# Kernel optimization log

Hardware: AMD Instinct MI355X
Metric: run time of the kernel (lower is better)

## Reference

```python
import jax, jax.numpy as jnp
import numpy as np

# torch.optim.Adam defaults
LR = 1e-3
B1 = 0.9
B2 = 0.999
EPS = 1e-8


def setup_inputs() -> dict:
    key = jax.random.key(0)
    k1, k2 = jax.random.split(key)
    B, N_train, d = 128, 16384, 1024
    h = jax.random.normal(k1, (B, d), dtype=jnp.float32)
    H_train = jax.random.normal(k2, (N_train, d), dtype=jnp.float32)
    return {"h": h, "H_train": H_train, "n_epoch": 1000}


def reference(h, H_train, n_epoch):
    # preweights: [B, N_train], optimized by Adam for n_epoch steps
    B, N_train = h.shape[0], H_train.shape[0]

    def loss_fn(p):
        w = jax.nn.softmax(p, axis=-1)          # [B, N_train]
        H_approx = w @ H_train                   # [B, d]
        return jnp.sum((H_approx - h) ** 2)

    grad_fn = jax.grad(loss_fn)

    def step(carry, t):
        p, m, v = carry
        g = grad_fn(p)
        m = B1 * m + (1.0 - B1) * g
        v = B2 * v + (1.0 - B2) * (g * g)
        m_hat = m / (1.0 - B1 ** t)
        v_hat = v / (1.0 - B2 ** t)
        p = p - LR * m_hat / (jnp.sqrt(v_hat) + EPS)
        return (p, m, v), None

    z = jnp.zeros((B, N_train), dtype=jnp.float32)
    ts = jnp.arange(1, n_epoch + 1, dtype=jnp.float32)
    (p, _, _), _ = jax.lax.scan(step, (z, z, z), ts)
    return jax.nn.softmax(p, axis=-1)
```

## Files before the change

### kernel.cpp

```cpp
#include <hip/hip_runtime.h>
#include <math.h>

#define BB 128
#define NTR 16384
#define DD 1024
#define PN (BB*NTR)
#define CN (BB*DD)
#define HN (NTR*DD)
#define FWD_SLABS 64
#define BWD_SLABS 2

typedef short bf16x8 __attribute__((ext_vector_type(8)));
typedef float f32x2  __attribute__((ext_vector_type(2)));
typedef float f32x4v __attribute__((ext_vector_type(4)));

__device__ __forceinline__ ushort f2bf(float f) {
  uint u = __float_as_uint(f);
  return (ushort)((u + 0x7FFFu + ((u >> 16) & 1u)) >> 16);
}
__device__ __forceinline__ float bf2f(ushort h) { return __uint_as_float(((uint)h) << 16); }
__device__ __forceinline__ void split2(float f, ushort& a, ushort& b) {
  a = f2bf(f); float r1 = f - bf2f(a);
  b = f2bf(r1);
}

__global__ __launch_bounds__(256) void k_prep(const float* __restrict__ H,
    ushort* __restrict__ H0, ushort* __restrict__ H1)
{
  const size_t i = ((size_t)blockIdx.x * 256 + threadIdx.x) * 4;
  const float4 x = *(const float4*)(H + i);
  ushort a[4], b[4];
  split2(x.x, a[0], b[0]); split2(x.y, a[1], b[1]);
  split2(x.z, a[2], b[2]); split2(x.w, a[3], b[3]);
  *(ushort4*)(H0 + i) = make_ushort4(a[0], a[1], a[2], a[3]);
  *(ushort4*)(H1 + i) = make_ushort4(b[0], b[1], b[2], b[3]);
}

__global__ __launch_bounds__(256) void k_stat0(float* __restrict__ pmx, float* __restrict__ psm) {
  const int i = blockIdx.x * 256 + threadIdx.x;
  pmx[i] = 0.f;
  psm[i] = 2048.f;
}

__device__ __forceinline__ void combine_stats(const float* __restrict__ pmx,
    const float* __restrict__ psm, int row, float& mx, float& inv)
{
  mx = -INFINITY;
#pragma unroll
  for (int c = 0; c < 8; ++c) mx = fmaxf(mx, pmx[c*128 + row]);
  float s = 0.f;
#pragma unroll
  for (int c = 0; c < 8; ++c) s += psm[c*128 + row] * expf(pmx[c*128 + row] - mx);
  inv = 1.0f / s;
}

__global__ __launch_bounds__(256) void k_wmat(const float* __restrict__ p,
    const float* __restrict__ pmx, const float* __restrict__ psm,
    float* __restrict__ w)
{
  const int bid = blockIdx.x, tid = threadIdx.x;
  const int row = bid >> 3;
  float mx, inv; combine_stats(pmx, psm, row, mx, inv);
  const size_t base = (size_t)bid * 2048 + tid * 8;
  const float4 a = *(const float4*)(p + base);
  const float4 b = *(const float4*)(p + base + 4);
  *(float4*)(w + base)     = make_float4(expf(a.x-mx)*inv, expf(a.y-mx)*inv,
                                         expf(a.z-mx)*inv, expf(a.w-mx)*inv);
  *(float4*)(w + base + 4) = make_float4(expf(b.x-mx)*inv, expf(b.y-mx)*inv,
                                         expf(b.z-mx)*inv, expf(b.w-mx)*inv);
}

__global__ __launch_bounds__(512) void k_softmax_f(const float* __restrict__ p,
                                                   float* __restrict__ w) {
  const int row = blockIdx.x, tid = threadIdx.x;
  const float* pr = p + (size_t)row * NTR;
  float x[32]; float mx = -INFINITY;
#pragma unroll
  for (int i = 0; i < 32; ++i) { x[i] = pr[i*512 + tid]; mx = fmaxf(mx, x[i]); }
  __shared__ float red[512];
  red[tid] = mx; __syncthreads();
  for (int s = 256; s > 0; s >>= 1) { if (tid < s) red[tid] = fmaxf(red[tid], red[tid+s]); __syncthreads(); }
  mx = red[0]; __syncthreads();
  float sum = 0.f;
#pragma unroll
  for (int i = 0; i < 32; ++i) { x[i] = expf(x[i] - mx); sum += x[i]; }
  red[tid] = sum; __syncthreads();
  for (int s = 256; s > 0; s >>= 1) { if (tid < s) red[tid] += red[tid+s]; __syncthreads(); }
  const float inv = 1.0f / red[0];
  float* wr = w + (size_t)row * NTR;
#pragma unroll
  for (int i = 0; i < 32; ++i) wr[i*512 + tid] = x[i] * inv;
}

__global__ __launch_bounds__(256) void k_fwd_v(const float* __restrict__ w,
    const float* __restrict__ H, float* __restrict__ Cp)
{
  const int nt = blockIdx.x, tid = threadIdx.x;
  const int kbase = blockIdx.y * 256;
  Cp += (size_t)blockIdx.y * CN;
  __shared__ float As[2][8][128];
  __shared__ float Bs[2][8][128];
  const int tm = tid >> 4, tn = tid & 15;
  const int m0 = tm * 8, n0 = tn * 8;
  const int mm = tid >> 1, q = tid & 1;
  const int br = tid >> 5, bc = (tid & 31) * 4;
  const float* Asrc = w + (size_t)mm*NTR + kbase + q*4;
  const float* Bsrc = H + (size_t)(kbase+br)*DD + nt*128 + bc;

  f32x2 acc[8][4];
#pragma unroll
  for (int i = 0; i < 8; ++i)
#pragma unroll
    for (int j = 0; j < 4; ++j) acc[i][j] = (f32x2){0.f, 0.f};

  float4 ra = *(const float4*)(Asrc);
  float4 rb = *(const float4*)(Bsrc);
  As[0][q*4+0][mm]=ra.x; As[0][q*4+1][mm]=ra.y; As[0][q*4+2][mm]=ra.z; As[0][q*4+3][mm]=ra.w;
  *(float4*)&Bs[0][br][bc] = rb;
  ra = *(const float4*)(Asrc + 8);
  rb = *(const float4*)(Bsrc + (size_t)8*DD);

  for (int t = 0; t < 32; ++t) {
    const int cur = t & 1;
    __syncthreads();
    if (t + 1 < 32) {
      As[cur^1][q*4+0][mm]=ra.x; As[cur^1][q*4+1][mm]=ra.y;
      As[cur^1][q*4+2][mm]=ra.z; As[cur^1][q*4+3][mm]=ra.w;
      *(float4*)&Bs[cur^1][br][bc] = rb;
    }
    if (t + 2 < 32) {
      ra = *(const float4*)(Asrc + (t+2)*8);
      rb = *(const float4*)(Bsrc + (size_t)((t+2)*8)*DD);
    }
#pragma unroll
    for (int k = 0; k < 8; ++k) {
      float a[8];
      *(float4*)&a[0] = *(const float4*)&As[cur][k][m0];
      *(float4*)&a[4] = *(const float4*)&As[cur][k][m0+4];
      f32x2 b[4];
      b[0] = *(const f32x2*)&Bs[cur][k][n0];
      b[1] = *(const f32x2*)&Bs[cur][k][n0+2];
      b[2] = *(const f32x2*)&Bs[cur][k][n0+4];
      b[3] = *(const f32x2*)&Bs[cur][k][n0+6];
#pragma unroll
      for (int i = 0; i < 8; ++i) {
        const f32x2 ai = (f32x2){a[i], a[i]};
#pragma unroll
        for (int j = 0; j < 4; ++j)
          acc[i][j] = __builtin_elementwise_fma(ai, b[j], acc[i][j]);
      }
    }
  }
#pragma unroll
  for (int i = 0; i < 8; ++i) {
    float* dst = Cp + (size_t)(m0+i)*DD + nt*128 + n0;
    *(float4*)dst     = make_float4(acc[i][0].x, acc[i][0].y, acc[i][1].x, acc[i][1].y);
    *(float4*)(dst+4) = make_float4(acc[i][2].x, acc[i][2].y, acc[i][3].x, acc[i][3].y);
  }
}

__global__ __launch_bounds__(256) void k_reduce_S2s(const float* __restrict__ X,
    const float* __restrict__ h,
    ushort* __restrict__ s0, ushort* __restrict__ s1)
{
  const size_t off = ((size_t)blockIdx.x * 256 + threadIdx.x) * 2;
  f32x2 s = (f32x2){0.f, 0.f};
#pragma unroll 4
  for (int k = 0; k < FWD_SLABS; ++k) {
    const f32x2 c = *(const f32x2*)(X + (size_t)k * CN + off);
    s.x += c.x; s.y += c.y;
  }
  const f32x2 hh = *(const f32x2*)(h + off);
  float v0 = 2.f*(s.x-hh.x), v1 = 2.f*(s.y-hh.y);
  ushort a0, b0, a1, b1;
  split2(v0, a0, b0); split2(v1, a1, b1);
  *(ushort2*)(s0 + off) = make_ushort2(a0, a1);
  *(ushort2*)(s1 + off) = make_ushort2(b0, b1);
}

__global__ __launch_bounds__(256, 2) void k_gemm3_bwd(
    const ushort* __restrict__ A0, const ushort* __restrict__ A1,
    const ushort* __restrict__ B0, const ushort* __restrict__ B1,
    const float* __restrict__ w,
    float* __restrict__ C, float* __restrict__ rpart)
{
  __shared__ ushort lds[12288];
  __shared__ float rbuf[128][33];
  const int tid = threadIdx.x;
  const int lane = tid & 63, wid = tid >> 6;
  const int wm = (wid >> 1) * 64, wn = (wid & 1) * 32;
  const int bn = blockIdx.x, ks = blockIdx.y;
  const int n0 = bn * 64;
  const int kbase = ks * 512;
  C += (size_t)ks * PN;

  const ushort* Ap[2] = {A0, A1};
  const ushort* Bp[2] = {B0, B1};

  f32x4v acc[4][2];
#pragma unroll
  for (int i = 0; i < 4; ++i)
#pragma unroll
    for (int j = 0; j < 2; ++j) acc[i][j] = (f32x4v){0.f, 0.f, 0.f, 0.f};

  for (int kt = 0; kt < 16; ++kt) {
    const int kpos = kbase + (kt << 5);
#pragma unroll
    for (int c = 0; c < 4; ++c) {
      const int L = c*256 + tid;
      const int s = L >> 9, rr = L & 511;
      const int row = rr >> 2, slot = rr & 3;
      const int sl = slot ^ ((row >> 1) & 3);
      const ushort* src = Ap[s] + (size_t)row * DD + kpos + (sl << 3);
      __builtin_amdgcn_global_load_lds((const __attribute__((address_space(1))) void*)src,
          (__attribute__((address_space(3))) void*)&lds[(size_t)(c*256 + (wid << 6)) * 8], 16, 0, 0);
    }
#pragma unroll
    for (int c = 0; c < 2; ++c) {
      const int L = c*256 + tid;
      const int s = L >> 8, rr = L & 255;
      const int row = rr >> 2, slot = rr & 3;
      const int sl = slot ^ ((row >> 1) & 3);
      const ushort* src = Bp[s] + (size_t)(n0 + row) * DD + kpos + (sl << 3);
      __builtin_amdgcn_global_load_lds((const __attribute__((address_space(1))) void*)src,
          (__attribute__((address_space(3))) void*)&lds[8192 + (size_t)(c*256 + (wid << 6)) * 8], 16, 0, 0);
    }
    __syncthreads();

    bf16x8 bf[2][2];
#pragma unroll
    for (int s = 0; s < 2; ++s)
#pragma unroll
      for (int j = 0; j < 2; ++j) {
        const int n = wn + j*16 + (lane & 15);
        const int sl = (lane >> 4) ^ ((n >> 1) & 3);
        bf[s][j] = *(const bf16x8*)&lds[8192 + s*2048 + n*32 + sl*8];
      }
#pragma unroll
    for (int sa = 0; sa < 2; ++sa) {
      bf16x8 af[4];
#pragma unroll
      for (int i = 0; i < 4; ++i) {
        const int mrow = wm + i*16 + (lane & 15);
        const int sl = (lane >> 4) ^ ((mrow >> 1) & 3);
        af[i] = *(const bf16x8*)&lds[sa*4096 + mrow*32 + sl*8];
      }
#pragma unroll
      for (int sb = 0; sb < 2 - sa; ++sb)
#pragma unroll
        for (int i = 0; i < 4; ++i)
#pragma unroll
          for (int j = 0; j < 2; ++j)
            acc[i][j] = __builtin_amdgcn_mfma_f32_16x16x32_bf16(af[i], bf[sb][j], acc[i][j], 0, 0, 0);
    }
    __syncthreads();
  }
#pragma unroll
  for (int i = 0; i < 4; ++i) {
    const int rbase = wm + i*16 + ((lane >> 4) << 2);
#pragma unroll
    for (int r = 0; r < 4; ++r) {
      const int row = rbase + r;
      float s = 0.f;
#pragma unroll
      for (int j = 0; j < 2; ++j) {
        const int cg = n0 + wn + j*16 + (lane & 15);
        C[(size_t)row * NTR + cg] = acc[i][j][r];
        s = fmaf(w[(size_t)row * NTR + cg], acc[i][j][r], s);
      }
      rbuf[row][((wn >> 5) << 4) + (lane & 15)] = s;
    }
  }
  __syncthreads();
  if (tid < 128) {
    float s = 0.f;
#pragma unroll
    for (int t = 0; t < 32; ++t) s += rbuf[tid][t];
    rpart[(size_t)tid * 512 + ks*256 + bn] = s;
  }
}

__global__ __launch_bounds__(256) void k_adam_f(float* __restrict__ pp_,
    float* __restrict__ m, float* __restrict__ v,
    const float* __restrict__ w, const float* __restrict__ X,
    const float* __restrict__ rpart,
    float* __restrict__ pmx_out, float* __restrict__ psm_out,
    float bc1, float bc2)
{
  const int bid = blockIdx.x, tid = threadIdx.x;
  const int row = bid >> 3, chunk = bid & 7;
  __shared__ float red[256];
  red[tid] = rpart[(size_t)row*512 + tid] + rpart[(size_t)row*512 + 256 + tid];
  __syncthreads();
  for (int s = 128; s > 0; s >>= 1) { if (tid < s) red[tid] += red[tid+s]; __syncthreads(); }
  const float rr = red[0];
  const size_t base = (size_t)bid * 2048 + tid * 4;
  float pn[8];
#pragma unroll
  for (int part = 0; part < 2; ++part) {
    const size_t off = base + part * 1024;
    float4 u  = *(const float4*)(X + off);
    const float4 u1 = *(const float4*)(X + (size_t)PN + off);
    u.x += u1.x; u.y += u1.y; u.z += u1.z; u.w += u1.w;
    const float4 w4 = *(const float4*)(w + off);
    const float wv[4] = {w4.x, w4.y, w4.z, w4.w};
    const float uu[4] = {u.x, u.y, u.z, u.w};
    float4 p4 = *(float4*)(pp_ + off);
    float4 m4 = *(float4*)(m + off);
    float4 v4 = *(float4*)(v + off);
    float* pp = (float*)&p4; float* mm = (float*)&m4; float* vv = (float*)&v4;
#pragma unroll
    for (int e = 0; e < 4; ++e) {
      const float g  = wv[e] * (uu[e] - rr);
      const float mn = 0.9f*mm[e] + 0.1f*g;
      const float vn = 0.999f*vv[e] + 0.001f*(g*g);
      const float mh = mn / bc1, vh = vn / bc2;
      pp[e] = pp[e] - 1e-3f * mh / (sqrtf(vh) + 1e-8f);
      mm[e] = mn; vv[e] = vn;
      pn[part*4 + e] = pp[e];
    }
    *(float4*)(pp_ + off) = p4;
    *(float4*)(m + off) = m4;
    *(float4*)(v + off) = v4;
  }
  float lmx = pn[0];
#pragma unroll
  for (int e = 1; e < 8; ++e) lmx = fmaxf(lmx, pn[e]);
  __syncthreads();
  red[tid] = lmx; __syncthreads();
  for (int s = 128; s > 0; s >>= 1) { if (tid < s) red[tid] = fmaxf(red[tid], red[tid+s]); __syncthreads(); }
  const float bmx = red[0]; __syncthreads();
  float ls = 0.f;
#pragma unroll
  for (int e = 0; e < 8; ++e) ls += expf(pn[e] - bmx);
  red[tid] = ls; __syncthreads();
  for (int s = 128; s > 0; s >>= 1) { if (tid < s) red[tid] += red[tid+s]; __syncthreads(); }
  if (tid == 0) {
    pmx_out[chunk*128 + row] = bmx;
    psm_out[chunk*128 + row] = red[0];
  }
}

extern "C" void kernel_launch(void* const* d_in, const int* in_sizes, int n_in,
                              void* d_out, int out_size, void* d_ws, size_t ws_size,
                              hipStream_t stream) {
  const float* h = (const float*)d_in[0];
  const float* H = (const float*)d_in[1];
  (void)in_sizes; (void)n_in; (void)out_size; (void)ws_size;
  const int n_epoch = 1000;

  float* p  = (float*)d_ws;
  float* m  = p + PN;
  float* v  = m + PN;
  float* w  = v + PN;
  float* X  = w + PN;
  float* rp = X + (size_t)4*PN;
  float* pmxA = rp + 128*512;
  float* psmA = pmxA + 1024;
  float* pmxB = psmA + 1024;
  float* psmB = pmxB + 1024;
  ushort* s0 = (ushort*)(psmB + 1024);
  ushort* s1 = s0 + CN;
  ushort* H0 = s1 + CN, *H1 = H0 + HN;

  hipMemsetAsync(p, 0, (size_t)3*PN*sizeof(float), stream);
  k_prep<<<HN/1024, 256, 0, stream>>>(H, H0, H1);
  k_stat0<<<4, 256, 0, stream>>>(pmxA, psmA);

  for (int s = 1; s <= n_epoch; ++s) {
    float* pmx_in  = (s & 1) ? pmxA : pmxB;
    float* psm_in  = (s & 1) ? psmA : psmB;
    float* pmx_out = (s & 1) ? pmxB : pmxA;
    float* psm_out = (s & 1) ? psmB : psmA;
    k_wmat<<<PN/2048, 256, 0, stream>>>(p, pmx_in, psm_in, w);
    k_fwd_v<<<dim3(8, FWD_SLABS), 256, 0, stream>>>(w, H, X);
    k_reduce_S2s<<<CN/512, 256, 0, stream>>>(X, h, s0, s1);
    k_gemm3_bwd<<<dim3(256, BWD_SLABS), 256, 0, stream>>>(s0, s1, H0, H1, w, X, rp);
    const float bc1 = 1.0f - powf(0.9f,   (float)s);
    const float bc2 = 1.0f - powf(0.999f, (float)s);
    k_adam_f<<<1024, 256, 0, stream>>>(p, m, v, w, X, rp, pmx_out, psm_out, bc1, bc2);
  }
  k_softmax_f<<<BB, 512, 0, stream>>>(p, (float*)d_out);
}
```

Before: 110.5 ms.

## Fuse softmax weight materialization into Adam by storing chunk-local exponentials

Removes the separate per-step k_wmat kernel. The Adam kernel now writes exp(p - chunk max) into a buffer, and the forward GEMM, backward GEMM and next Adam step rebuild the softmax weights on the fly from the per-chunk max/sum stats. This saves one full read of p and one write of w (a 128x16384 fp32 matrix) plus a launch every step. In exchange, each consumer block recomputes the row scale factors, and the forward B-tile LDS reads were merged into float4 loads.

```diff
diff --git a/kernel.cpp b/kernel.cpp
--- a/kernel.cpp
+++ b/kernel.cpp
@@ -41,6 +41,12 @@
   pmx[i] = 0.f;
   psm[i] = 2048.f;
 }
+__global__ __launch_bounds__(256) void k_einit(float* __restrict__ e) {
+  const size_t base = (size_t)blockIdx.x * 2048 + threadIdx.x * 8;
+  const float4 one = make_float4(1.f, 1.f, 1.f, 1.f);
+  *(float4*)(e + base) = one;
+  *(float4*)(e + base + 4) = one;
+}
 
 __device__ __forceinline__ void combine_stats(const float* __restrict__ pmx,
     const float* __restrict__ psm, int row, float& mx, float& inv)
@@ -52,22 +58,6 @@
 #pragma unroll
   for (int c = 0; c < 8; ++c) s += psm[c*128 + row] * expf(pmx[c*128 + row] - mx);
   inv = 1.0f / s;
-}
-
-__global__ __launch_bounds__(256) void k_wmat(const float* __restrict__ p,
-    const float* __restrict__ pmx, const float* __restrict__ psm,
-    float* __restrict__ w)
-{
-  const int bid = blockIdx.x, tid = threadIdx.x;
-  const int row = bid >> 3;
-  float mx, inv; combine_stats(pmx, psm, row, mx, inv);
-  const size_t base = (size_t)bid * 2048 + tid * 8;
-  const float4 a = *(const float4*)(p + base);
-  const float4 b = *(const float4*)(p + base + 4);
-  *(float4*)(w + base)     = make_float4(expf(a.x-mx)*inv, expf(a.y-mx)*inv,
-                                         expf(a.z-mx)*inv, expf(a.w-mx)*inv);
-  *(float4*)(w + base + 4) = make_float4(expf(b.x-mx)*inv, expf(b.y-mx)*inv,
-                                         expf(b.z-mx)*inv, expf(b.w-mx)*inv);
 }
 
 __global__ __launch_bounds__(512) void k_softmax_f(const float* __restrict__ p,
@@ -92,20 +82,29 @@
   for (int i = 0; i < 32; ++i) wr[i*512 + tid] = x[i] * inv;
 }
 
-__global__ __launch_bounds__(256) void k_fwd_v(const float* __restrict__ w,
+__global__ __launch_bounds__(256) void k_fwd_v(const float* __restrict__ e,
+    const float* __restrict__ pmx, const float* __restrict__ psm,
     const float* __restrict__ H, float* __restrict__ Cp)
 {
   const int nt = blockIdx.x, tid = threadIdx.x;
   const int kbase = blockIdx.y * 256;
+  const int chunk = kbase >> 11;
   Cp += (size_t)blockIdx.y * CN;
   __shared__ float As[2][8][128];
   __shared__ float Bs[2][8][128];
+  __shared__ float sscale[128];
+  if (tid < 128) {
+    float mx, inv; combine_stats(pmx, psm, tid, mx, inv);
+    sscale[tid] = expf(pmx[chunk*128 + tid] - mx) * inv;
+  }
   const int tm = tid >> 4, tn = tid & 15;
   const int m0 = tm * 8, n0 = tn * 8;
   const int mm = tid >> 1, q = tid & 1;
   const int br = tid >> 5, bc = (tid & 31) * 4;
-  const float* Asrc = w + (size_t)mm*NTR + kbase + q*4;
+  const float* Asrc = e + (size_t)mm*NTR + kbase + q*4;
   const float* Bsrc = H + (size_t)(kbase+br)*DD + nt*128 + bc;
+  __syncthreads();
+  const float sA = sscale[mm];
 
   f32x2 acc[8][4];
 #pragma unroll
@@ -115,7 +114,8 @@
 
   float4 ra = *(const float4*)(Asrc);
   float4 rb = *(const float4*)(Bsrc);
-  As[0][q*4+0][mm]=ra.x; As[0][q*4+1][mm]=ra.y; As[0][q*4+2][mm]=ra.z; As[0][q*4+3][mm]=ra.w;
+  As[0][q*4+0][mm]=ra.x*sA; As[0][q*4+1][mm]=ra.y*sA;
+  As[0][q*4+2][mm]=ra.z*sA; As[0][q*4+3][mm]=ra.w*sA;
   *(float4*)&Bs[0][br][bc] = rb;
   ra = *(const float4*)(Asrc + 8);
   rb = *(const float4*)(Bsrc + (size_t)8*DD);
@@ -124,8 +124,8 @@
     const int cur = t & 1;
     __syncthreads();
     if (t + 1 < 32) {
-      As[cur^1][q*4+0][mm]=ra.x; As[cur^1][q*4+1][mm]=ra.y;
-      As[cur^1][q*4+2][mm]=ra.z; As[cur^1][q*4+3][mm]=ra.w;
+      As[cur^1][q*4+0][mm]=ra.x*sA; As[cur^1][q*4+1][mm]=ra.y*sA;
+      As[cur^1][q*4+2][mm]=ra.z*sA; As[cur^1][q*4+3][mm]=ra.w*sA;
       *(float4*)&Bs[cur^1][br][bc] = rb;
     }
     if (t + 2 < 32) {
@@ -137,11 +137,11 @@
       float a[8];
       *(float4*)&a[0] = *(const float4*)&As[cur][k][m0];
       *(float4*)&a[4] = *(const float4*)&As[cur][k][m0+4];
+      const float4 b01 = *(const float4*)&Bs[cur][k][n0];
+      const float4 b23 = *(const float4*)&Bs[cur][k][n0+4];
       f32x2 b[4];
-      b[0] = *(const f32x2*)&Bs[cur][k][n0];
-      b[1] = *(const f32x2*)&Bs[cur][k][n0+2];
-      b[2] = *(const f32x2*)&Bs[cur][k][n0+4];
-      b[3] = *(const f32x2*)&Bs[cur][k][n0+6];
+      b[0] = (f32x2){b01.x, b01.y}; b[1] = (f32x2){b01.z, b01.w};
+      b[2] = (f32x2){b23.x, b23.y}; b[3] = (f32x2){b23.z, b23.w};
 #pragma unroll
       for (int i = 0; i < 8; ++i) {
         const f32x2 ai = (f32x2){a[i], a[i]};
@@ -181,18 +181,26 @@
 __global__ __launch_bounds__(256, 2) void k_gemm3_bwd(
     const ushort* __restrict__ A0, const ushort* __restrict__ A1,
     const ushort* __restrict__ B0, const ushort* __restrict__ B1,
-    const float* __restrict__ w,
+    const float* __restrict__ e,
+    const float* __restrict__ pmx, const float* __restrict__ psm,
     float* __restrict__ C, float* __restrict__ rpart)
 {
   __shared__ ushort lds[12288];
   __shared__ float rbuf[128][33];
+  __shared__ float sscale[128];
   const int tid = threadIdx.x;
   const int lane = tid & 63, wid = tid >> 6;
   const int wm = (wid >> 1) * 64, wn = (wid & 1) * 32;
   const int bn = blockIdx.x, ks = blockIdx.y;
   const int n0 = bn * 64;
+  const int chunk = n0 >> 11;
   const int kbase = ks * 512;
   C += (size_t)ks * PN;
+
+  if (tid < 128) {
+    float mx, inv; combine_stats(pmx, psm, tid, mx, inv);
+    sscale[tid] = expf(pmx[chunk*128 + tid] - mx) * inv;
+  }
 
   const ushort* Ap[2] = {A0, A1};
   const ushort* Bp[2] = {B0, B1};
@@ -261,12 +269,13 @@
 #pragma unroll
     for (int r = 0; r < 4; ++r) {
       const int row = rbase + r;
+      const float sc = sscale[row];
       float s = 0.f;
 #pragma unroll
       for (int j = 0; j < 2; ++j) {
         const int cg = n0 + wn + j*16 + (lane & 15);
         C[(size_t)row * NTR + cg] = acc[i][j][r];
-        s = fmaf(w[(size_t)row * NTR + cg], acc[i][j][r], s);
+        s = fmaf(e[(size_t)row * NTR + cg] * sc, acc[i][j][r], s);
       }
       rbuf[row][((wn >> 5) << 4) + (lane & 15)] = s;
     }
@@ -282,13 +291,16 @@
 
 __global__ __launch_bounds__(256) void k_adam_f(float* __restrict__ pp_,
     float* __restrict__ m, float* __restrict__ v,
-    const float* __restrict__ w, const float* __restrict__ X,
+    float* __restrict__ e, const float* __restrict__ X,
     const float* __restrict__ rpart,
+    const float* __restrict__ pmx_in, const float* __restrict__ psm_in,
     float* __restrict__ pmx_out, float* __restrict__ psm_out,
     float bc1, float bc2)
 {
   const int bid = blockIdx.x, tid = threadIdx.x;
   const int row = bid >> 3, chunk = bid & 7;
+  float mx, inv; combine_stats(pmx_in, psm_in, row, mx, inv);
+  const float sc = expf(pmx_in[chunk*128 + row] - mx) * inv;
   __shared__ float red[256];
   red[tid] = rpart[(size_t)row*512 + tid] + rpart[(size_t)row*512 + 256 + tid];
   __syncthreads();
@@ -302,22 +314,22 @@
     float4 u  = *(const float4*)(X + off);
     const float4 u1 = *(const float4*)(X + (size_t)PN + off);
     u.x += u1.x; u.y += u1.y; u.z += u1.z; u.w += u1.w;
-    const float4 w4 = *(const float4*)(w + off);
-    const float wv[4] = {w4.x, w4.y, w4.z, w4.w};
+    const float4 e4 = *(const float4*)(e + off);
+    const float wv[4] = {e4.x*sc, e4.y*sc, e4.z*sc, e4.w*sc};
     const float uu[4] = {u.x, u.y, u.z, u.w};
     float4 p4 = *(float4*)(pp_ + off);
     float4 m4 = *(float4*)(m + off);
     float4 v4 = *(float4*)(v + off);
     float* pp = (float*)&p4; float* mm = (float*)&m4; float* vv = (float*)&v4;
 #pragma unroll
-    for (int e = 0; e < 4; ++e) {
-      const float g  = wv[e] * (uu[e] - rr);
-      const float mn = 0.9f*mm[e] + 0.1f*g;
-      const float vn = 0.999f*vv[e] + 0.001f*(g*g);
+    for (int e2 = 0; e2 < 4; ++e2) {
+      const float g  = wv[e2] * (uu[e2] - rr);
+      const float mn = 0.9f*mm[e2] + 0.1f*g;
+      const float vn = 0.999f*vv[e2] + 0.001f*(g*g);
       const float mh = mn / bc1, vh = vn / bc2;
-      pp[e] = pp[e] - 1e-3f * mh / (sqrtf(vh) + 1e-8f);
-      mm[e] = mn; vv[e] = vn;
-      pn[part*4 + e] = pp[e];
+      pp[e2] = pp[e2] - 1e-3f * mh / (sqrtf(vh) + 1e-8f);
+      mm[e2] = mn; vv[e2] = vn;
+      pn[part*4 + e2] = pp[e2];
     }
     *(float4*)(pp_ + off) = p4;
     *(float4*)(m + off) = m4;
@@ -325,14 +337,20 @@
   }
   float lmx = pn[0];
 #pragma unroll
-  for (int e = 1; e < 8; ++e) lmx = fmaxf(lmx, pn[e]);
+  for (int e2 = 1; e2 < 8; ++e2) lmx = fmaxf(lmx, pn[e2]);
   __syncthreads();
   red[tid] = lmx; __syncthreads();
   for (int s = 128; s > 0; s >>= 1) { if (tid < s) red[tid] = fmaxf(red[tid], red[tid+s]); __syncthreads(); }
   const float bmx = red[0]; __syncthreads();
+  float en[8];
   float ls = 0.f;
 #pragma unroll
-  for (int e = 0; e < 8; ++e) ls += expf(pn[e] - bmx);
+  for (int e2 = 0; e2 < 8; ++e2) { en[e2] = expf(pn[e2] - bmx); ls += en[e2]; }
+#pragma unroll
+  for (int part = 0; part < 2; ++part) {
+    const size_t off = base + part * 1024;
+    *(float4*)(e + off) = make_float4(en[part*4+0], en[part*4+1], en[part*4+2], en[part*4+3]);
+  }
   red[tid] = ls; __syncthreads();
   for (int s = 128; s > 0; s >>= 1) { if (tid < s) red[tid] += red[tid+s]; __syncthreads(); }
   if (tid == 0) {
@@ -352,8 +370,8 @@
   float* p  = (float*)d_ws;
   float* m  = p + PN;
   float* v  = m + PN;
-  float* w  = v + PN;
-  float* X  = w + PN;
+  float* e  = v + PN;
+  float* X  = e + PN;
   float* rp = X + (size_t)4*PN;
   float* pmxA = rp + 128*512;
   float* psmA = pmxA + 1024;
@@ -366,19 +384,19 @@
   hipMemsetAsync(p, 0, (size_t)3*PN*sizeof(float), stream);
   k_prep<<<HN/1024, 256, 0, stream>>>(H, H0, H1);
   k_stat0<<<4, 256, 0, stream>>>(pmxA, psmA);
+  k_einit<<<PN/2048, 256, 0, stream>>>(e);
 
   for (int s = 1; s <= n_epoch; ++s) {
     float* pmx_in  = (s & 1) ? pmxA : pmxB;
     float* psm_in  = (s & 1) ? psmA : psmB;
     float* pmx_out = (s & 1) ? pmxB : pmxA;
     float* psm_out = (s & 1) ? psmB : psmA;
-    k_wmat<<<PN/2048, 256, 0, stream>>>(p, pmx_in, psm_in, w);
-    k_fwd_v<<<dim3(8, FWD_SLABS), 256, 0, stream>>>(w, H, X);
+    k_fwd_v<<<dim3(8, FWD_SLABS), 256, 0, stream>>>(e, pmx_in, psm_in, H, X);
     k_reduce_S2s<<<CN/512, 256, 0, stream>>>(X, h, s0, s1);
-    k_gemm3_bwd<<<dim3(256, BWD_SLABS), 256, 0, stream>>>(s0, s1, H0, H1, w, X, rp);
+    k_gemm3_bwd<<<dim3(256, BWD_SLABS), 256, 0, stream>>>(s0, s1, H0, H1, e, pmx_in, psm_in, X, rp);
     const float bc1 = 1.0f - powf(0.9f,   (float)s);
     const float bc2 = 1.0f - powf(0.999f, (float)s);
-    k_adam_f<<<1024, 256, 0, stream>>>(p, m, v, w, X, rp, pmx_out, psm_out, bc1, bc2);
+    k_adam_f<<<1024, 256, 0, stream>>>(p, m, v, e, X, rp, pmx_in, psm_in, pmx_out, psm_out, bc1, bc2);
   }
   k_softmax_f<<<BB, 512, 0, stream>>>(p, (float*)d_out);
 }
```

New measurement: 107.6 ms (median of 2 runs). -2.6%, faster.
